# Kernel optimization log

Hardware: AMD Instinct MI355X
Metric: run time of the kernel (lower is better)

## Reference

```python
import jax, jax.numpy as jnp
import numpy as np


def setup_inputs() -> dict:
    key = jax.random.key(0)
    ks = jax.random.split(key, 7)
    B, Sq, St, E = 4, 2048, 2048, 512
    s = E ** -0.5
    return {
        "query": jax.random.normal(ks[0], (B, Sq, E), jnp.float32),
        "target": jax.random.normal(ks[1], (B, St, E), jnp.float32),
        "bias": jax.random.normal(ks[2], (1, 1, Sq, St), jnp.float32),
        "Wq": jax.random.normal(ks[3], (E, E), jnp.float32) * s,
        "Wk": jax.random.normal(ks[4], (E, E), jnp.float32) * s,
        "Wv": jax.random.normal(ks[5], (E, E), jnp.float32) * s,
        "Wo": jax.random.normal(ks[6], (E, E), jnp.float32) * s,
    }


def reference(query, target, bias, Wq, Wk, Wv, Wo):
    B, Sq, E = query.shape
    St = target.shape[1]
    H = 8
    hd = E // H  # head_size

    q = query @ Wq   # [B, Sq, E]
    k = target @ Wk  # [B, St, E]
    v = target @ Wv  # [B, St, E]

    # split heads: [B, S, E] -> [B, H, S, hd]
    q = q.reshape(B, Sq, H, hd).transpose(0, 2, 1, 3)
    k = k.reshape(B, St, H, hd).transpose(0, 2, 1, 3)
    v = v.reshape(B, St, H, hd).transpose(0, 2, 1, 3)

    # scores: [B, H, Sq, St]
    weight = jnp.einsum('bhqd,bhtd->bhqt', q, k) / jnp.sqrt(jnp.float32(hd))
    weight = weight + bias
    weight = jax.nn.softmax(weight, axis=-1)
    # dropout: inference mode (training=False) -> identity

    out = jnp.einsum('bhqt,bhtd->bhqd', weight, v)  # [B, H, Sq, hd]
    out = out.transpose(0, 2, 1, 3).reshape(B, Sq, E)  # merge heads
    return out @ Wo
```

## Files before the change

### kernel.cpp

```cpp
#include <hip/hip_runtime.h>
#include <cstdint>

#define B_ 4
#define SQ_ 2048
#define ST_ 2048
#define E_ 512
#define H_ 8
#define HD_ 64
#define LDQ_ (3 * E_)
#define QS_ 0.18033688011112043f
#define L2E_ 1.44269504089f
#define BC_ 14.0f

typedef _Float16 f16_t;
typedef _Float16 f16x8 __attribute__((ext_vector_type(8)));
typedef _Float16 f16x4 __attribute__((ext_vector_type(4)));
typedef float f32x4 __attribute__((ext_vector_type(4)));

static __device__ __forceinline__ f16x8 ld8(const f16_t* p) {
  return *reinterpret_cast<const f16x8*>(p);
}

static __device__ __forceinline__ void gld16(const f16_t* g, f16_t* l) {
  __builtin_amdgcn_global_load_lds((const __attribute__((address_space(1))) void*)g,
                                   (__attribute__((address_space(3))) void*)l, 16, 0, 0);
}

static __device__ __forceinline__ int swz(int row, int ch) {
  return row * 64 + (((ch ^ (row & 7)) & 7) << 3);
}

__global__ __launch_bounds__(256) void preproc_kernel(const float* __restrict__ query,
                                                      const float* __restrict__ target,
                                                      const float* __restrict__ bias,
                                                      const float* __restrict__ Wq,
                                                      const float* __restrict__ Wk,
                                                      const float* __restrict__ Wv,
                                                      const float* __restrict__ Wo,
                                                      f16_t* __restrict__ qb,
                                                      f16_t* __restrict__ tb,
                                                      f16x4* __restrict__ biasRT,
                                                      f16_t* __restrict__ WqkvT,
                                                      f16_t* __restrict__ WoT) {
  __shared__ float smem[64 * 65];
  const int g = blockIdx.x;
  const int tid = threadIdx.x;
  if (g < 8192) {
    const int n4 = (B_ * SQ_ * E_) / 4;
    int i = g * 256 + tid;
    const float* in = query;
    f16_t* out = qb;
    if (i >= n4) { i -= n4; in = target; out = tb; }
    float4 v = reinterpret_cast<const float4*>(in)[i];
    f16x4 o = {(f16_t)v.x, (f16_t)v.y, (f16_t)v.z, (f16_t)v.w};
    reinterpret_cast<f16x4*>(out)[i] = o;
  } else if (g < 9216) {
    const int gb = g - 8192;
    const int t0 = (gb & 31) * 64;
    const int q0 = (gb >> 5) * 64;
    for (int i = tid; i < 64 * 64; i += 256) {
      const int q = i >> 6, t = i & 63;
      smem[q * 65 + t] = bias[(size_t)(q0 + q) * ST_ + t0 + t];
    }
    __syncthreads();
#pragma unroll
    for (int s = 0; s < 4; ++s) {
      const int slot = s * 256 + tid;
      const int tile_id = slot >> 6;
      const int lane = slot & 63;
      const int tq = tile_id >> 2, tt = tile_id & 3;
      const int quad = lane >> 4, l16 = lane & 15;
      f16x4 v;
#pragma unroll
      for (int r = 0; r < 4; ++r)
        v[r] = (f16_t)(smem[(tq * 16 + l16) * 65 + tt * 16 + quad * 4 + r] * L2E_ - BC_);
      const size_t qb16 = (q0 >> 4) + tq, tb16 = (t0 >> 4) + tt;
      biasRT[(qb16 * 128 + tb16) * 64 + lane] = v;
    }
  } else {
    const int gw = g - 9216;
    const int w = gw >> 8;
    const float* W = (w == 0) ? Wq : (w == 1) ? Wk : (w == 2) ? Wv : Wo;
    f16_t* Wt = (w < 3) ? WqkvT + (size_t)w * E_ * E_ : WoT;
    const float sc = (w == 0) ? QS_ : 1.0f;
    const int bx = (gw & 15) * 32;
    const int by = ((gw >> 4) & 15) * 32;
    const int tx = tid & 31;
    const int ty = tid >> 5;
#pragma unroll
    for (int i = 0; i < 4; ++i)
      smem[(ty + i * 8) * 33 + tx] = W[(size_t)(by + ty + i * 8) * E_ + bx + tx];
    __syncthreads();
#pragma unroll
    for (int i = 0; i < 4; ++i)
      Wt[(size_t)(bx + ty + i * 8) * E_ + by + tx] = (f16_t)(smem[tx * 33 + ty + i * 8] * sc);
  }
}

__global__ __launch_bounds__(256) void vtrans_kernel(const f16_t* __restrict__ Vsrc,
                                                     f16_t* __restrict__ VT) {
  __shared__ f16_t tile[64][72];
  const int bh = blockIdx.y;
  const int b = bh >> 3, h = bh & 7;
  const int t0 = blockIdx.x * 64;
  for (int i = threadIdx.x; i < 64 * 64; i += 256) {
    const int t = i >> 6, d = i & 63;
    tile[d][t] = Vsrc[(size_t)(b * ST_ + t0 + t) * LDQ_ + h * HD_ + d];
  }
  __syncthreads();
  for (int i = threadIdx.x; i < 64 * 64; i += 256) {
    const int d = i >> 6, t = i & 63;
    VT[(size_t)(bh * HD_ + d) * ST_ + t0 + t] = tile[d][t];
  }
}

template <bool OUT_F16>
__global__ __launch_bounds__(256) void gemm_bt2_kernel(const f16_t* __restrict__ Aq,
                                                       const f16_t* __restrict__ Akv,
                                                       const f16_t* __restrict__ Bt,
                                                       void* __restrict__ Cv,
                                                       int K, int ldc) {
  __shared__ f16_t As[128 * 32];
  __shared__ f16_t Bs[128 * 32];
  const int tid = threadIdx.x;
  const int lane = tid & 63;
  const int wave = tid >> 6;
  const int wm = (wave >> 1) * 64;
  const int wn = (wave & 1) * 64;
  const int m0 = blockIdx.y * 128;
  const int n0 = blockIdx.x * 128;
  const int l16 = lane & 15;
  const int quad = lane >> 4;
  const f16_t* A = (n0 < E_) ? Aq : Akv;

  f32x4 acc[4][4] = {};

  const int r0 = wave * 16 + (lane >> 2);
  const int r1 = (wave + 4) * 16 + (lane >> 2);
  const int c0 = (lane & 3) * 8;
  const f16_t* Ag0 = A + (size_t)(m0 + r0) * K + c0;
  const f16_t* Ag1 = A + (size_t)(m0 + r1) * K + c0;
  const f16_t* Bg0 = Bt + (size_t)(n0 + r0) * K + c0;
  const f16_t* Bg1 = Bt + (size_t)(n0 + r1) * K + c0;
  f16_t* Al0 = &As[wave * 512 + lane * 8];
  f16_t* Al1 = &As[(wave + 4) * 512 + lane * 8];
  f16_t* Bl0 = &Bs[wave * 512 + lane * 8];
  f16_t* Bl1 = &Bs[(wave + 4) * 512 + lane * 8];

  for (int k0 = 0; k0 < K; k0 += 32) {
    __syncthreads();
    gld16(Ag0 + k0, Al0);
    gld16(Ag1 + k0, Al1);
    gld16(Bg0 + k0, Bl0);
    gld16(Bg1 + k0, Bl1);
    __syncthreads();
    f16x8 af[4], bfr[4];
#pragma unroll
    for (int i = 0; i < 4; ++i) af[i] = ld8(&As[(wm + i * 16 + l16) * 32 + quad * 8]);
#pragma unroll
    for (int j = 0; j < 4; ++j) bfr[j] = ld8(&Bs[(wn + j * 16 + l16) * 32 + quad * 8]);
#pragma unroll
    for (int i = 0; i < 4; ++i)
#pragma unroll
      for (int j = 0; j < 4; ++j)
        acc[i][j] = __builtin_amdgcn_mfma_f32_16x16x32_f16(af[i], bfr[j], acc[i][j], 0, 0, 0);
  }

#pragma unroll
  for (int i = 0; i < 4; ++i)
#pragma unroll
    for (int r = 0; r < 4; ++r) {
      const size_t row = (size_t)m0 + wm + i * 16 + quad * 4 + r;
#pragma unroll
      for (int j = 0; j < 4; ++j) {
        const size_t col = (size_t)n0 + wn + j * 16 + l16;
        if (OUT_F16)
          reinterpret_cast<f16_t*>(Cv)[row * (size_t)ldc + col] = (f16_t)acc[i][j][r];
        else
          reinterpret_cast<float*>(Cv)[row * (size_t)ldc + col] = acc[i][j][r];
      }
    }
}

__global__ __launch_bounds__(256, 4) void attn_kernel(const f16_t* __restrict__ QKV,
                                                      const f16_t* __restrict__ VT,
                                                      const f16x4* __restrict__ biasRT,
                                                      f16_t* __restrict__ O) {
  __shared__ f16_t Ks[64 * 64];
  __shared__ f16_t Vs[64 * 64];
  __shared__ f16_t Ps[4][16][72];
  const int id = blockIdx.x;
  const int bh = id & 31;
  const int b = bh >> 3, h = bh & 7;
  const int q0 = (id >> 5) * 64;
  const int tid = threadIdx.x;
  const int wave = tid >> 6;
  const int lane = tid & 63;
  const int l16 = lane & 15;
  const int quad = lane >> 4;
  const int qw = q0 + wave * 16;

  const f16_t* qptr = QKV + (size_t)(b * SQ_ + qw + l16) * LDQ_ + h * HD_ + quad * 8;
  const f16x8 bq0 = ld8(qptr);
  const f16x8 bq1 = ld8(qptr + 32);

  const int ch0 = wave * 2, ch1 = ch0 + 1;
  const int rsub = lane >> 3;
  const int csub = (((lane & 7) ^ (lane >> 3)) << 3);
  const f16_t* kg0 = QKV + (size_t)(b * ST_ + ch0 * 8 + rsub) * LDQ_ + E_ + h * HD_ + csub;
  const f16_t* kg1 = QKV + (size_t)(b * ST_ + ch1 * 8 + rsub) * LDQ_ + E_ + h * HD_ + csub;
  const f16_t* vg0 = VT + (size_t)(bh * HD_ + ch0 * 8 + rsub) * ST_ + csub;
  const f16_t* vg1 = VT + (size_t)(bh * HD_ + ch1 * 8 + rsub) * ST_ + csub;
  f16_t* kl0 = &Ks[ch0 * 512 + lane * 8];
  f16_t* kl1 = &Ks[ch1 * 512 + lane * 8];
  f16_t* vl0 = &Vs[ch0 * 512 + lane * 8];
  f16_t* vl1 = &Vs[ch1 * 512 + lane * 8];

  const f16x4* bRT = biasRT + (size_t)(qw >> 4) * 128 * 64 + lane;

  f16x4 nb[4];
#pragma unroll
  for (int tt = 0; tt < 4; ++tt) nb[tt] = bRT[(size_t)tt * 64];

  f32x4 facc[4] = {};
  float l_i = 0.f;

  for (int t0 = 0; t0 < ST_; t0 += 64) {
    __syncthreads();
    gld16(kg0, kl0);
    gld16(kg1, kl1);
    gld16(vg0, vl0);
    gld16(vg1, vl1);
    kg0 += 64 * LDQ_;
    kg1 += 64 * LDQ_;
    vg0 += 64;
    vg1 += 64;
    f32x4 cb[4];
#pragma unroll
    for (int tt = 0; tt < 4; ++tt)
#pragma unroll
      for (int r = 0; r < 4; ++r) cb[tt][r] = (float)nb[tt][r];
    __syncthreads();

    if (t0 + 64 < ST_) {
      const f16x4* bn = bRT + (size_t)((t0 + 64) >> 4) * 64;
#pragma unroll
      for (int tt = 0; tt < 4; ++tt) nb[tt] = bn[(size_t)tt * 64];
    }

    f32x4 s[4];
#pragma unroll
    for (int tt = 0; tt < 4; ++tt) {
      const int row = tt * 16 + l16;
      f32x4 a = cb[tt];
      a = __builtin_amdgcn_mfma_f32_16x16x32_f16(ld8(&Ks[swz(row, quad)]), bq0, a, 0, 0, 0);
      a = __builtin_amdgcn_mfma_f32_16x16x32_f16(ld8(&Ks[swz(row, quad + 4)]), bq1, a, 0, 0, 0);
      s[tt] = a;
    }

#pragma unroll
    for (int tt = 0; tt < 4; ++tt) {
      f16x4 pk;
#pragma unroll
      for (int r = 0; r < 4; ++r) {
        const float pv = exp2f(s[tt][r]);
        l_i += pv;
        pk[r] = (f16_t)pv;
      }
      *reinterpret_cast<f16x4*>(&Ps[wave][l16][tt * 16 + quad * 4]) = pk;
    }

#pragma unroll
    for (int tc = 0; tc < 2; ++tc) {
      const f16x8 ap = ld8(&Ps[wave][l16][tc * 32 + quad * 8]);
#pragma unroll
      for (int j = 0; j < 4; ++j) {
        const f16x8 bv = ld8(&Vs[swz(j * 16 + l16, tc * 4 + quad)]);
        facc[j] = __builtin_amdgcn_mfma_f32_16x16x32_f16(ap, bv, facc[j], 0, 0, 0);
      }
    }
  }

  l_i += __shfl_xor(l_i, 16);
  l_i += __shfl_xor(l_i, 32);
#pragma unroll
  for (int r = 0; r < 4; ++r) {
    const float lr = __shfl(l_i, quad * 4 + r);
    const float inv = 1.0f / lr;
    f16_t* op = O + (size_t)(b * SQ_ + qw + quad * 4 + r) * E_ + h * HD_ + l16;
#pragma unroll
    for (int j = 0; j < 4; ++j) op[j * 16] = (f16_t)(facc[j][r] * inv);
  }
}

extern "C" void kernel_launch(void* const* d_in, const int* in_sizes, int n_in,
                              void* d_out, int out_size, void* d_ws, size_t ws_size,
                              hipStream_t stream) {
  (void)in_sizes; (void)n_in; (void)out_size; (void)ws_size;
  const float* query = (const float*)d_in[0];
  const float* target = (const float*)d_in[1];
  const float* bias = (const float*)d_in[2];
  const float* Wq = (const float*)d_in[3];
  const float* Wk = (const float*)d_in[4];
  const float* Wv = (const float*)d_in[5];
  const float* Wo = (const float*)d_in[6];

  char* ws = (char*)d_ws;
  const size_t ACT = (size_t)B_ * SQ_ * E_;
  const size_t ACT_B = ACT * sizeof(f16_t);
  const size_t BIAS_B = (size_t)SQ_ * ST_ * sizeof(f16_t);
  const size_t W_B = (size_t)E_ * E_ * sizeof(f16_t);

  f16_t* qb = (f16_t*)(ws);
  f16_t* tb = (f16_t*)(ws + ACT_B);
  f16_t* biasRT = (f16_t*)(ws + 2 * ACT_B);
  f16_t* WqkvT = (f16_t*)(ws + 2 * ACT_B + BIAS_B);
  f16_t* WoT = WqkvT + 3 * (size_t)E_ * E_;
  f16_t* QKV = (f16_t*)(ws + 2 * ACT_B + BIAS_B + 4 * W_B);
  f16_t* VT = qb;
  f16_t* attn = tb;

  dim3 blk(256);
  preproc_kernel<<<dim3(10240), blk, 0, stream>>>(query, target, bias, Wq, Wk, Wv, Wo, qb, tb,
                                                  (f16x4*)biasRT, WqkvT, WoT);

  gemm_bt2_kernel<true><<<dim3(3 * E_ / 128, B_ * SQ_ / 128), blk, 0, stream>>>(
      qb, tb, WqkvT, QKV, E_, LDQ_);

  vtrans_kernel<<<dim3(ST_ / 64, B_ * H_), blk, 0, stream>>>(QKV + 2 * E_, VT);

  attn_kernel<<<dim3(SQ_ / 64 * B_ * H_), blk, 0, stream>>>(QKV, VT, (const f16x4*)biasRT, attn);

  gemm_bt2_kernel<false><<<dim3(E_ / 128, B_ * SQ_ / 128), blk, 0, stream>>>(
      attn, attn, WoT, (void*)d_out, E_, E_);
}
```

Baseline: 222.1 us.

## Double-buffer K/V tiles in attention loop, use raw v_exp, relayout P scratch

The attention kernel now keeps two LDS buffers for K and V. The next 64-key tile is issued with global_load_lds while the current tile is being computed, so load latency can overlap the MFMA work. exp2f is replaced with a raw v_exp_f32 inline asm. The per-wave P scratch is relaid into unpadded 8-element chunks, and the row-sum now accumulates in a vector. LDS use roughly doubles and may limit occupancy, and correctness relies on the barriers covering the async LDS writes.

```diff
diff --git a/kernel.cpp b/kernel.cpp
--- a/kernel.cpp
+++ b/kernel.cpp
@@ -19,6 +19,12 @@
 
 static __device__ __forceinline__ f16x8 ld8(const f16_t* p) {
   return *reinterpret_cast<const f16x8*>(p);
+}
+
+static __device__ __forceinline__ float fast_exp2(float x) {
+  float r;
+  asm("v_exp_f32 %0, %1" : "=v"(r) : "v"(x));
+  return r;
 }
 
 static __device__ __forceinline__ void gld16(const f16_t* g, f16_t* l) {
@@ -186,9 +192,9 @@
                                                       const f16_t* __restrict__ VT,
                                                       const f16x4* __restrict__ biasRT,
                                                       f16_t* __restrict__ O) {
-  __shared__ f16_t Ks[64 * 64];
-  __shared__ f16_t Vs[64 * 64];
-  __shared__ f16_t Ps[4][16][72];
+  __shared__ f16_t Ks[2][64 * 64];
+  __shared__ f16_t Vs[2][64 * 64];
+  __shared__ f16_t Ps[4][1024];
   const int id = blockIdx.x;
   const int bh = id & 31;
   const int b = bh >> 3, h = bh & 7;
@@ -211,76 +217,97 @@
   const f16_t* kg1 = QKV + (size_t)(b * ST_ + ch1 * 8 + rsub) * LDQ_ + E_ + h * HD_ + csub;
   const f16_t* vg0 = VT + (size_t)(bh * HD_ + ch0 * 8 + rsub) * ST_ + csub;
   const f16_t* vg1 = VT + (size_t)(bh * HD_ + ch1 * 8 + rsub) * ST_ + csub;
-  f16_t* kl0 = &Ks[ch0 * 512 + lane * 8];
-  f16_t* kl1 = &Ks[ch1 * 512 + lane * 8];
-  f16_t* vl0 = &Vs[ch0 * 512 + lane * 8];
-  f16_t* vl1 = &Vs[ch1 * 512 + lane * 8];
+  const int loff0 = ch0 * 512 + lane * 8;
+  const int loff1 = ch1 * 512 + lane * 8;
 
   const f16x4* bRT = biasRT + (size_t)(qw >> 4) * 128 * 64 + lane;
 
+  gld16(kg0, &Ks[0][loff0]);
+  gld16(kg1, &Ks[0][loff1]);
+  gld16(vg0, &Vs[0][loff0]);
+  gld16(vg1, &Vs[0][loff1]);
+  kg0 += 64 * LDQ_;
+  kg1 += 64 * LDQ_;
+  vg0 += 64;
+  vg1 += 64;
   f16x4 nb[4];
 #pragma unroll
   for (int tt = 0; tt < 4; ++tt) nb[tt] = bRT[(size_t)tt * 64];
 
   f32x4 facc[4] = {};
-  float l_i = 0.f;
+  f32x4 lacc = {};
+  int cur = 0;
+  __syncthreads();
 
   for (int t0 = 0; t0 < ST_; t0 += 64) {
-    __syncthreads();
-    gld16(kg0, kl0);
-    gld16(kg1, kl1);
-    gld16(vg0, vl0);
-    gld16(vg1, vl1);
-    kg0 += 64 * LDQ_;
-    kg1 += 64 * LDQ_;
-    vg0 += 64;
-    vg1 += 64;
-    f32x4 cb[4];
-#pragma unroll
-    for (int tt = 0; tt < 4; ++tt)
-#pragma unroll
-      for (int r = 0; r < 4; ++r) cb[tt][r] = (float)nb[tt][r];
-    __syncthreads();
-
+    const int nxt = cur ^ 1;
+    f16x4 nbn[4];
     if (t0 + 64 < ST_) {
+      gld16(kg0, &Ks[nxt][loff0]);
+      gld16(kg1, &Ks[nxt][loff1]);
+      gld16(vg0, &Vs[nxt][loff0]);
+      gld16(vg1, &Vs[nxt][loff1]);
+      kg0 += 64 * LDQ_;
+      kg1 += 64 * LDQ_;
+      vg0 += 64;
+      vg1 += 64;
       const f16x4* bn = bRT + (size_t)((t0 + 64) >> 4) * 64;
 #pragma unroll
-      for (int tt = 0; tt < 4; ++tt) nb[tt] = bn[(size_t)tt * 64];
+      for (int tt = 0; tt < 4; ++tt) nbn[tt] = bn[(size_t)tt * 64];
     }
 
     f32x4 s[4];
 #pragma unroll
     for (int tt = 0; tt < 4; ++tt) {
       const int row = tt * 16 + l16;
-      f32x4 a = cb[tt];
-      a = __builtin_amdgcn_mfma_f32_16x16x32_f16(ld8(&Ks[swz(row, quad)]), bq0, a, 0, 0, 0);
-      a = __builtin_amdgcn_mfma_f32_16x16x32_f16(ld8(&Ks[swz(row, quad + 4)]), bq1, a, 0, 0, 0);
+      f32x4 a;
+#pragma unroll
+      for (int r = 0; r < 4; ++r) a[r] = (float)nb[tt][r];
+      a = __builtin_amdgcn_mfma_f32_16x16x32_f16(ld8(&Ks[cur][swz(row, quad)]), bq0, a, 0, 0, 0);
+      a = __builtin_amdgcn_mfma_f32_16x16x32_f16(ld8(&Ks[cur][swz(row, quad + 4)]), bq1, a, 0, 0, 0);
       s[tt] = a;
     }
 
+    f16x4 pk[4];
 #pragma unroll
     for (int tt = 0; tt < 4; ++tt) {
-      f16x4 pk;
 #pragma unroll
       for (int r = 0; r < 4; ++r) {
-        const float pv = exp2f(s[tt][r]);
-        l_i += pv;
-        pk[r] = (f16_t)pv;
+        const float pv = fast_exp2(s[tt][r]);
+        lacc[r] += pv;
+        pk[tt][r] = (f16_t)pv;
       }
-      *reinterpret_cast<f16x4*>(&Ps[wave][l16][tt * 16 + quad * 4]) = pk;
+    }
+
+    __syncthreads();
+
+    f16_t* psb = Ps[wave];
+#pragma unroll
+    for (int tt = 0; tt < 4; ++tt) {
+      const int p = tt * 2 + (quad >> 1);
+      *reinterpret_cast<f16x4*>(&psb[(p * 16 + l16) * 8 + (quad & 1) * 4]) = pk[tt];
     }
 
 #pragma unroll
     for (int tc = 0; tc < 2; ++tc) {
-      const f16x8 ap = ld8(&Ps[wave][l16][tc * 32 + quad * 8]);
+      const f16x8 ap = ld8(&psb[((tc * 4 + quad) * 16 + l16) * 8]);
 #pragma unroll
       for (int j = 0; j < 4; ++j) {
-        const f16x8 bv = ld8(&Vs[swz(j * 16 + l16, tc * 4 + quad)]);
+        const f16x8 bv = ld8(&Vs[cur][swz(j * 16 + l16, tc * 4 + quad)]);
         facc[j] = __builtin_amdgcn_mfma_f32_16x16x32_f16(ap, bv, facc[j], 0, 0, 0);
       }
     }
-  }
-
+
+    __syncthreads();
+
+    if (t0 + 64 < ST_) {
+#pragma unroll
+      for (int tt = 0; tt < 4; ++tt) nb[tt] = nbn[tt];
+    }
+    cur = nxt;
+  }
+
+  float l_i = lacc[0] + lacc[1] + lacc[2] + lacc[3];
   l_i += __shfl_xor(l_i, 16);
   l_i += __shfl_xor(l_i, 32);
 #pragma unroll
```

After: 213.1 us. 4.1% less time.
